# Kernel optimization log

Measured on AMD Instinct MI355X. Metric: run time of the kernel, lower is better.

Reference implementation:

```python
import jax, jax.numpy as jnp
import numpy as np

ENT_TYPE_SIZE = 9
INNER_DIM = 64
NEG_INF = 1e12


def _rope_interleaved(x, cos_pos, sin_pos):
    # x: (B, S, H, D); rotate interleaved pairs: (x0,x1)->(x0*c - x1*s, x1*c + x0*s)
    x2 = jnp.stack([-x[..., 1::2], x[..., ::2]], axis=-1).reshape(x.shape)
    return x * cos_pos + x2 * sin_pos


def setup_inputs() -> dict:
    key = jax.random.key(0)
    k1, k2 = jax.random.split(key)
    B, S, H = 16, 512, 768
    out_dim = ENT_TYPE_SIZE * INNER_DIM * 2  # 1152
    last_hidden_state = jax.random.normal(k1, (B, S, H), dtype=jnp.float32)
    attention_mask = jnp.ones((B, S), dtype=jnp.float32)
    W_dense = jax.random.normal(k2, (H, out_dim), dtype=jnp.float32) * (1.0 / np.sqrt(H))
    b_dense = jnp.zeros((out_dim,), dtype=jnp.float32)
    return {
        "last_hidden_state": last_hidden_state,
        "attention_mask": attention_mask,
        "W_dense": W_dense,
        "b_dense": b_dense,
    }


def reference(last_hidden_state, attention_mask, W_dense, b_dense):
    B, S, H = last_hidden_state.shape
    ent, inner = ENT_TYPE_SIZE, INNER_DIM

    # dense projection then split into per-entity-type q/k vectors
    proj = last_hidden_state @ W_dense + b_dense            # (B, S, ent*2*inner)
    proj = proj.reshape(B, S, ent, 2 * inner)
    qw, kw = proj[..., :inner], proj[..., inner:]           # (B, S, ent, inner)

    # inline RoPE, interleaved sin/cos layout per sinusoidal_position_embedding
    pos = jnp.arange(S, dtype=jnp.float32)[:, None]         # (S, 1)
    idx = jnp.arange(inner // 2, dtype=jnp.float32)
    freqs = pos * jnp.power(10000.0, -2.0 * idx / inner)    # (S, inner/2)
    cos_pos = jnp.repeat(jnp.cos(freqs), 2, axis=-1)[None, :, None, :]  # (1,S,1,inner)
    sin_pos = jnp.repeat(jnp.sin(freqs), 2, axis=-1)[None, :, None, :]
    qw = _rope_interleaved(qw, cos_pos, sin_pos)
    kw = _rope_interleaved(kw, cos_pos, sin_pos)

    # pairwise span scores
    logits = jnp.einsum('bmhd,bnhd->bhmn', qw, kw)          # (B, ent, S, S)

    # padding mask on key positions (canonical GlobalPointer masking)
    pad = attention_mask[:, None, None, :]                  # (B,1,1,S)
    logits = logits * pad - (1.0 - pad) * NEG_INF

    # strict lower triangle masked out (only spans with start <= end)
    tril = jnp.tril(jnp.ones((S, S), dtype=logits.dtype), -1)
    logits = logits - tril * NEG_INF

    return logits / (inner ** 0.5)
```

## Files before the change

kernel.cpp:

```cpp
#include <hip/hip_runtime.h>
#include <hip/hip_bf16.h>
#include <cstdint>

typedef __bf16 bf8 __attribute__((ext_vector_type(8)));
typedef __bf16 bf4 __attribute__((ext_vector_type(4)));
typedef float  f4  __attribute__((ext_vector_type(4)));

typedef const void __attribute__((address_space(1)))* as1_cvp;
typedef void       __attribute__((address_space(3)))* as3_vp;

#define NEG_INF_F 1000000000000.0f

__device__ __forceinline__ void lds_load16(const __bf16* g, __bf16* l) {
    __builtin_amdgcn_global_load_lds((as1_cvp)g, (as3_vp)l, 16, 0, 0);
}

__device__ __forceinline__ void gemm_tile_core(
    const __bf16* __restrict__ Atile, const __bf16* __restrict__ Btile,
    int lda, int ldb, int Ktot,
    __bf16* sA, __bf16* sB, f4 acc[4][4])
{
    const int t    = threadIdx.x;
    const int wave = t >> 6;
    const int lane = t & 63;
    const int quad = lane >> 4;
    const int m16  = lane & 15;
    const int wm   = (wave >> 1) * 64;
    const int wn   = (wave & 1) * 64;

    for (int k0 = 0; k0 < Ktot; k0 += 32) {
        __syncthreads();
#pragma unroll
        for (int i = 0; i < 2; ++i) {
            const int f   = i * 256 + t;
            const int row = f >> 2;
            const int ch  = (f & 3) * 8;
            lds_load16(Atile + (size_t)row * lda + k0 + ch,
                       sA + (i * 256 + wave * 64) * 8);
            lds_load16(Btile + (size_t)row * ldb + k0 + ch,
                       sB + (i * 256 + wave * 64) * 8);
        }
        __syncthreads();

        bf8 af[4], bfr[4];
#pragma unroll
        for (int mi = 0; mi < 4; ++mi)
            af[mi] = *(const bf8*)(sA + (wm + mi * 16 + m16) * 32 + quad * 8);
#pragma unroll
        for (int ni = 0; ni < 4; ++ni)
            bfr[ni] = *(const bf8*)(sB + (wn + ni * 16 + m16) * 32 + quad * 8);
#pragma unroll
        for (int mi = 0; mi < 4; ++mi)
#pragma unroll
            for (int ni = 0; ni < 4; ++ni)
                acc[mi][ni] = __builtin_amdgcn_mfma_f32_16x16x32_bf16(
                    af[mi], bfr[ni], acc[mi][ni], 0, 0, 0);
    }
}

__global__ __launch_bounds__(256) void cast_a_kernel(
    const float* __restrict__ in, __bf16* __restrict__ out, int n4)
{
    int idx = blockIdx.x * 256 + threadIdx.x;
    if (idx < n4) {
        const float4 v = reinterpret_cast<const float4*>(in)[idx];
        bf4 o = { (__bf16)v.x, (__bf16)v.y, (__bf16)v.z, (__bf16)v.w };
        reinterpret_cast<bf4*>(out)[idx] = o;
    }
}

__global__ __launch_bounds__(256) void transpose_w_kernel(
    const float* __restrict__ W, __bf16* __restrict__ Wt)
{
    __shared__ __bf16 tile[32][33];
    const int n0 = blockIdx.x * 32;
    const int k0 = blockIdx.y * 32;
    const int tx = threadIdx.x & 31;
    const int ty = threadIdx.x >> 5;
#pragma unroll
    for (int r = 0; r < 32; r += 8)
        tile[ty + r][tx] = (__bf16)W[(size_t)(k0 + ty + r) * 1152 + n0 + tx];
    __syncthreads();
#pragma unroll
    for (int r = 0; r < 32; r += 8)
        Wt[(size_t)(n0 + ty + r) * 768 + k0 + tx] = tile[tx][ty + r];
}

__global__ __launch_bounds__(256) void proj_rope_kernel(
    const __bf16* __restrict__ A,
    const __bf16* __restrict__ Wt,
    const float*  __restrict__ bias,
    __bf16* __restrict__ qbuf, __bf16* __restrict__ kbuf)
{
    __shared__ __bf16 sA[128 * 32];
    __shared__ __bf16 sB[128 * 32];
    f4 acc[4][4] = {};

    const int rowTile = blockIdx.y * 128;
    const int colTile = blockIdx.x * 128;
    gemm_tile_core(A + (size_t)rowTile * 768, Wt + (size_t)colTile * 768,
                   768, 768, 768, sA, sB, acc);

    const int t = threadIdx.x, wave = t >> 6, lane = t & 63;
    const int quad = lane >> 4, m16 = lane & 15;
    const int wm = (wave >> 1) * 64, wn = (wave & 1) * 64;

#pragma unroll
    for (int ni = 0; ni < 4; ++ni) {
        const int gc = colTile + wn + ni * 16 + m16;
        const float bv = bias[gc];
        const int e  = gc >> 7;
        const int d  = gc & 63;
        const int qk = (gc >> 6) & 1;
        const float theta = exp2f((float)(d >> 1) * -0.4152410118609203f);
        const float sgn = (d & 1) ? 1.0f : -1.0f;
        __bf16* dst = qk ? kbuf : qbuf;
#pragma unroll
        for (int mi = 0; mi < 4; ++mi) {
#pragma unroll
            for (int r = 0; r < 4; ++r) {
                const int gm = rowTile + wm + mi * 16 + quad * 4 + r;
                const int bb = gm >> 9;
                const int s  = gm & 511;
                float v = acc[mi][ni][r] + bv;
                float p = __shfl_xor(v, 1);
                float sn, cs;
                __sincosf((float)s * theta, &sn, &cs);
                float o = v * cs + sgn * p * sn;
                dst[(size_t)(((bb * 9 + e) * 512 + s)) * 64 + d] = (__bf16)o;
            }
        }
    }
}

__global__ __launch_bounds__(256, 3) void logits_kernel(
    const __bf16* __restrict__ qbuf, const __bf16* __restrict__ kbuf,
    const float* __restrict__ amask, float* __restrict__ out)
{
    __shared__ __bf16 sQ[2 * 128 * 32];
    __shared__ __bf16 sK[2][2 * 128 * 32];

    const int t    = threadIdx.x;
    const int wave = t >> 6;
    const int lane = t & 63;
    const int quad = lane >> 4;
    const int m16  = lane & 15;
    const int wm   = (wave >> 1) * 64;
    const int wn   = (wave & 1) * 64;

    const int be = blockIdx.y;
    const int b  = be / 9;
    const int rowTile = blockIdx.x * 128;
    const __bf16* Qg = qbuf + (size_t)be * 512 * 64 + (size_t)rowTile * 64;
    const __bf16* Kg = kbuf + (size_t)be * 512 * 64;

#pragma unroll
    for (int i = 0; i < 4; ++i) {
        const int l = i * 256 + t;
        const int p = l >> 9;
        const int r = (l >> 2) & 127;
        const int j = l & 3;
        const int g = r * 8 + p * 4 + j;
        lds_load16(Qg + g * 8, sQ + (i * 256 + wave * 64) * 8);
        lds_load16(Kg + g * 8, sK[0] + (i * 256 + wave * 64) * 8);
    }
    __syncthreads();

    for (int c = 0; c < 4; ++c) {
        if (c < 3) {
            const __bf16* Kc = Kg + (size_t)(c + 1) * 128 * 64;
            __bf16* dstb = sK[(c + 1) & 1];
#pragma unroll
            for (int i = 0; i < 4; ++i) {
                const int l = i * 256 + t;
                const int p = l >> 9;
                const int r = (l >> 2) & 127;
                const int j = l & 3;
                const int g = r * 8 + p * 4 + j;
                lds_load16(Kc + g * 8, dstb + (i * 256 + wave * 64) * 8);
            }
        }

        const __bf16* sKc = sK[c & 1];
        f4 acc[4][4] = {};
#pragma unroll
        for (int kp = 0; kp < 2; ++kp) {
            bf8 af[4], bfr[4];
#pragma unroll
            for (int mi = 0; mi < 4; ++mi)
                af[mi] = *(const bf8*)(sQ + kp * 4096 + (wm + mi * 16 + m16) * 32 + quad * 8);
#pragma unroll
            for (int ni = 0; ni < 4; ++ni)
                bfr[ni] = *(const bf8*)(sKc + kp * 4096 + (wn + ni * 16 + m16) * 32 + quad * 8);
#pragma unroll
            for (int mi = 0; mi < 4; ++mi)
#pragma unroll
                for (int ni = 0; ni < 4; ++ni)
                    acc[mi][ni] = __builtin_amdgcn_mfma_f32_16x16x32_bf16(
                        af[mi], bfr[ni], acc[mi][ni], 0, 0, 0);
        }

        const int colTile = c * 128;
#pragma unroll
        for (int ni = 0; ni < 4; ++ni) {
            const int n = colTile + wn + ni * 16 + m16;
            const float pad    = amask[b * 512 + n];
            const float padoff = (1.0f - pad) * NEG_INF_F;
#pragma unroll
            for (int mi = 0; mi < 4; ++mi) {
#pragma unroll
                for (int r = 0; r < 4; ++r) {
                    const int m = rowTile + wm + mi * 16 + quad * 4 + r;
                    float v = acc[mi][ni][r] * pad - padoff;
                    if (n < m) v -= NEG_INF_F;
                    out[((size_t)(be * 512 + m) << 9) + n] = v * 0.125f;
                }
            }
        }
        __syncthreads();
    }
}

extern "C" void kernel_launch(void* const* d_in, const int* in_sizes, int n_in,
                              void* d_out, int out_size, void* d_ws, size_t ws_size,
                              hipStream_t stream) {
    const float* lhs   = (const float*)d_in[0];
    const float* amask = (const float*)d_in[1];
    const float* W     = (const float*)d_in[2];
    const float* bias  = (const float*)d_in[3];
    float* out = (float*)d_out;

    char* ws = (char*)d_ws;
    __bf16* Abf = (__bf16*)ws;
    __bf16* Wt  = (__bf16*)(ws + 12582912);
    __bf16* qb  = (__bf16*)(ws + 14352384);
    __bf16* kb  = (__bf16*)(ws + 23789568);

    cast_a_kernel<<<6144, 256, 0, stream>>>(lhs, Abf, 1572864);
    transpose_w_kernel<<<dim3(36, 24), 256, 0, stream>>>(W, Wt);
    proj_rope_kernel<<<dim3(9, 64), 256, 0, stream>>>(Abf, Wt, bias, qb, kb);
    logits_kernel<<<dim3(4, 144), 256, 0, stream>>>(qb, kb, amask, out);
}
```

Before: 227.3 us.

## Merge cast and transpose kernels, precompute RoPE table, simplify projection epilogue

Result: no change. 227.6 us (+0.1%).

```diff
diff --git a/kernel.cpp b/kernel.cpp
--- a/kernel.cpp
+++ b/kernel.cpp
@@ -58,38 +58,47 @@
     }
 }
 
-__global__ __launch_bounds__(256) void cast_a_kernel(
-    const float* __restrict__ in, __bf16* __restrict__ out, int n4)
-{
-    int idx = blockIdx.x * 256 + threadIdx.x;
-    if (idx < n4) {
+__global__ __launch_bounds__(256) void prep_kernel(
+    const float* __restrict__ in, __bf16* __restrict__ Abf,
+    const float* __restrict__ W, __bf16* __restrict__ Wt,
+    float2* __restrict__ rope)
+{
+    __shared__ __bf16 tile[32][33];
+    const int bx = blockIdx.x;
+    if (bx < 6144) {
+        const int idx = bx * 256 + threadIdx.x;
         const float4 v = reinterpret_cast<const float4*>(in)[idx];
         bf4 o = { (__bf16)v.x, (__bf16)v.y, (__bf16)v.z, (__bf16)v.w };
-        reinterpret_cast<bf4*>(out)[idx] = o;
-    }
-}
-
-__global__ __launch_bounds__(256) void transpose_w_kernel(
-    const float* __restrict__ W, __bf16* __restrict__ Wt)
-{
-    __shared__ __bf16 tile[32][33];
-    const int n0 = blockIdx.x * 32;
-    const int k0 = blockIdx.y * 32;
-    const int tx = threadIdx.x & 31;
-    const int ty = threadIdx.x >> 5;
-#pragma unroll
-    for (int r = 0; r < 32; r += 8)
-        tile[ty + r][tx] = (__bf16)W[(size_t)(k0 + ty + r) * 1152 + n0 + tx];
-    __syncthreads();
-#pragma unroll
-    for (int r = 0; r < 32; r += 8)
-        Wt[(size_t)(n0 + ty + r) * 768 + k0 + tx] = tile[tx][ty + r];
+        reinterpret_cast<bf4*>(Abf)[idx] = o;
+    } else if (bx < 7008) {
+        const int b2 = bx - 6144;
+        const int n0 = (b2 % 36) * 32;
+        const int k0 = (b2 / 36) * 32;
+        const int tx = threadIdx.x & 31;
+        const int ty = threadIdx.x >> 5;
+#pragma unroll
+        for (int r = 0; r < 32; r += 8)
+            tile[ty + r][tx] = (__bf16)W[(size_t)(k0 + ty + r) * 1152 + n0 + tx];
+        __syncthreads();
+#pragma unroll
+        for (int r = 0; r < 32; r += 8)
+            Wt[(size_t)(n0 + ty + r) * 768 + k0 + tx] = tile[tx][ty + r];
+    } else {
+        const int idx = (bx - 7008) * 256 + threadIdx.x;
+        const int s = idx >> 6;
+        const int d = idx & 63;
+        const float theta = exp2f((float)(d >> 1) * -0.4152410118609203f);
+        float sn, cs;
+        __sincosf((float)s * theta, &sn, &cs);
+        rope[idx] = make_float2(cs, (d & 1) ? sn : -sn);
+    }
 }
 
 __global__ __launch_bounds__(256) void proj_rope_kernel(
     const __bf16* __restrict__ A,
     const __bf16* __restrict__ Wt,
     const float*  __restrict__ bias,
+    const float2* __restrict__ rope,
     __bf16* __restrict__ qbuf, __bf16* __restrict__ kbuf)
 {
     __shared__ __bf16 sA[128 * 32];
@@ -105,29 +114,26 @@
     const int quad = lane >> 4, m16 = lane & 15;
     const int wm = (wave >> 1) * 64, wn = (wave & 1) * 64;
 
+    const int e  = colTile >> 7;
+    const int bb = rowTile >> 9;
+    const int sbase = (rowTile & 511) + wm + quad * 4;
+    __bf16* dst0 = (wave & 1) ? kbuf : qbuf;
+    __bf16* dst  = dst0 + (size_t)(bb * 9 + e) * 512 * 64;
+
 #pragma unroll
     for (int ni = 0; ni < 4; ++ni) {
-        const int gc = colTile + wn + ni * 16 + m16;
-        const float bv = bias[gc];
-        const int e  = gc >> 7;
-        const int d  = gc & 63;
-        const int qk = (gc >> 6) & 1;
-        const float theta = exp2f((float)(d >> 1) * -0.4152410118609203f);
-        const float sgn = (d & 1) ? 1.0f : -1.0f;
-        __bf16* dst = qk ? kbuf : qbuf;
+        const int d  = ni * 16 + m16;
+        const float bv = bias[colTile + wn + d];
 #pragma unroll
         for (int mi = 0; mi < 4; ++mi) {
 #pragma unroll
             for (int r = 0; r < 4; ++r) {
-                const int gm = rowTile + wm + mi * 16 + quad * 4 + r;
-                const int bb = gm >> 9;
-                const int s  = gm & 511;
+                const int s = sbase + mi * 16 + r;
                 float v = acc[mi][ni][r] + bv;
                 float p = __shfl_xor(v, 1);
-                float sn, cs;
-                __sincosf((float)s * theta, &sn, &cs);
-                float o = v * cs + sgn * p * sn;
-                dst[(size_t)(((bb * 9 + e) * 512 + s)) * 64 + d] = (__bf16)o;
+                const float2 tt = rope[s * 64 + d];
+                float o = v * tt.x + p * tt.y;
+                dst[(size_t)s * 64 + d] = (__bf16)o;
             }
         }
     }
@@ -231,13 +237,13 @@
     float* out = (float*)d_out;
 
     char* ws = (char*)d_ws;
-    __bf16* Abf = (__bf16*)ws;
-    __bf16* Wt  = (__bf16*)(ws + 12582912);
-    __bf16* qb  = (__bf16*)(ws + 14352384);
-    __bf16* kb  = (__bf16*)(ws + 23789568);
-
-    cast_a_kernel<<<6144, 256, 0, stream>>>(lhs, Abf, 1572864);
-    transpose_w_kernel<<<dim3(36, 24), 256, 0, stream>>>(W, Wt);
-    proj_rope_kernel<<<dim3(9, 64), 256, 0, stream>>>(Abf, Wt, bias, qb, kb);
+    __bf16* Abf  = (__bf16*)ws;
+    __bf16* Wt   = (__bf16*)(ws + 12582912);
+    __bf16* qb   = (__bf16*)(ws + 14352384);
+    __bf16* kb   = (__bf16*)(ws + 23789568);
+    float2* rope = (float2*)(ws + 33226752);
+
+    prep_kernel<<<7136, 256, 0, stream>>>(lhs, Abf, W, Wt, rope);
+    proj_rope_kernel<<<dim3(9, 64), 256, 0, stream>>>(Abf, Wt, bias, rope, qb, kb);
     logits_kernel<<<dim3(4, 144), 256, 0, stream>>>(qb, kb, amask, out);
 }
```
